# Performance work log

Hardware: AMD Instinct MI355X
Metric: run time of the kernel (lower is better)

## Reference

```python
import jax, jax.numpy as jnp
import numpy as np

N = 100000
E = 1600000
IN_DIM = 4
HIDDEN = 64
OUT = 32
HEADS = 4
NEG_SLOPE = 0.2


def setup_inputs() -> dict:
    key = jax.random.key(0)
    ks = jax.random.split(key, 12)
    C1 = HIDDEN // HEADS  # 16 per-head channels in conv1
    inp = {
        "x": jax.random.normal(ks[0], (N, IN_DIM), dtype=jnp.float32),
        "edge_index": jax.random.randint(ks[1], (2, E), 0, N, dtype=jnp.int64),
        # conv1 (GATv2, heads=4, out_channels=16, concat)
        "Wl1": jax.random.normal(ks[2], (IN_DIM, HEADS * C1), dtype=jnp.float32) * 0.3,
        "Wr1": jax.random.normal(ks[3], (IN_DIM, HEADS * C1), dtype=jnp.float32) * 0.3,
        "att1": jax.random.normal(ks[4], (HEADS, C1), dtype=jnp.float32) * 0.3,
        "b1": jax.random.normal(ks[5], (HEADS * C1,), dtype=jnp.float32) * 0.1,
        "g1": jnp.ones((HIDDEN,), dtype=jnp.float32),
        "be1": jnp.zeros((HIDDEN,), dtype=jnp.float32),
        # conv2 (GATv2, heads=1, out_channels=32)
        "Wl2": jax.random.normal(ks[6], (HIDDEN, OUT), dtype=jnp.float32) * 0.1,
        "Wr2": jax.random.normal(ks[7], (HIDDEN, OUT), dtype=jnp.float32) * 0.1,
        "att2": jax.random.normal(ks[8], (1, OUT), dtype=jnp.float32) * 0.3,
        "b2": jax.random.normal(ks[9], (OUT,), dtype=jnp.float32) * 0.1,
        "g2": jnp.ones((OUT,), dtype=jnp.float32),
        "be2": jnp.zeros((OUT,), dtype=jnp.float32),
    }
    return inp


def gatv2_conv(x, Wl, Wr, att, bias, src, dst, heads, out_ch):
    # x: [N, F_in]; lin_l for source messages, lin_r for target (PyG GATv2Conv defaults)
    xl = (x @ Wl).reshape(N, heads, out_ch)  # [N,H,C]
    xr = (x @ Wr).reshape(N, heads, out_ch)
    m = xl[src] + xr[dst]                                     # [E,H,C] gather
    e = jnp.sum(jax.nn.leaky_relu(m, NEG_SLOPE) * att, axis=-1)  # [E,H]
    # segment softmax over destination node
    emax = jax.ops.segment_max(e, dst, num_segments=N)        # [N,H]
    ee = jnp.exp(e - emax[dst])
    denom = jax.ops.segment_sum(ee, dst, num_segments=N)      # [N,H]
    alpha = ee / denom[dst]
    out = jax.ops.segment_sum(xl[src] * alpha[..., None], dst, num_segments=N)  # [N,H,C]
    return out.reshape(N, heads * out_ch) + bias


def layer_norm(x, gamma, beta, eps=1e-5):
    mu = jnp.mean(x, axis=-1, keepdims=True)
    var = jnp.var(x, axis=-1, keepdims=True)
    return (x - mu) * jax.lax.rsqrt(var + eps) * gamma + beta


def reference(x, edge_index, Wl1, Wr1, att1, b1, g1, be1, Wl2, Wr2, att2, b2, g2, be2):
    src, dst = edge_index[0], edge_index[1]
    h = gatv2_conv(x, Wl1, Wr1, att1, b1, src, dst, HEADS, HIDDEN // HEADS)
    h = jax.nn.elu(layer_norm(h, g1, be1))
    h = gatv2_conv(h, Wl2, Wr2, att2, b2, src, dst, 1, OUT)
    return layer_norm(h, g2, be2)
```

## Files before the change

### kernel.cpp

```cpp
#include <hip/hip_runtime.h>
#include <math.h>

#define NN 100000
#define NE 1600000
#define HID 64
#define OUTC 32
#define NBUCK 196
#define NPB 512
#define EPB 3125
#define MAXB 10240
#define LOG2E 1.44269504088896340736f

typedef float f32x2 __attribute__((ext_vector_type(2)));

__device__ __forceinline__ f32x2 pk_mul(f32x2 a, f32x2 b) {
    f32x2 r;
    asm("v_pk_mul_f32 %0, %1, %2" : "=v"(r) : "v"(a), "v"(b));
    return r;
}
__device__ __forceinline__ f32x2 pk_fma(f32x2 a, f32x2 b, f32x2 c) {
    f32x2 r;
    asm("v_pk_fma_f32 %0, %1, %2, %3" : "=v"(r) : "v"(a), "v"(b), "v"(c));
    return r;
}
__device__ __forceinline__ f32x2 pk_add(f32x2 a, f32x2 b) {
    f32x2 r;
    asm("v_pk_add_f32 %0, %1, %2" : "=v"(r) : "v"(a), "v"(b));
    return r;
}
__device__ __forceinline__ f32x2 pk_fma_blo(f32x2 x, f32x2 b, f32x2 c) {
    f32x2 r;
    asm("v_pk_fma_f32 %0, %1, %2, %3 op_sel:[0,0,0] op_sel_hi:[0,1,1]" : "=v"(r) : "v"(x), "v"(b), "v"(c));
    return r;
}
__device__ __forceinline__ f32x2 pk_fma_bhi(f32x2 x, f32x2 b, f32x2 c) {
    f32x2 r;
    asm("v_pk_fma_f32 %0, %1, %2, %3 op_sel:[1,0,0] op_sel_hi:[1,1,1]" : "=v"(r) : "v"(x), "v"(b), "v"(c));
    return r;
}
__device__ __forceinline__ f32x2 pk_mul_bhi(f32x2 x, f32x2 b) {
    f32x2 r;
    asm("v_pk_mul_f32 %0, %1, %2 op_sel:[1,0] op_sel_hi:[1,1]" : "=v"(r) : "v"(x), "v"(b));
    return r;
}
__device__ __forceinline__ f32x2 pk_abs(f32x2 a) {
    f32x2 r;
    r.x = __builtin_fabsf(a.x);
    r.y = __builtin_fabsf(a.y);
    return r;
}
__device__ __forceinline__ unsigned short f2bf(float f) {
    unsigned int u = __float_as_uint(f);
    u += 0x7FFFu + ((u >> 16) & 1u);
    return (unsigned short)(u >> 16);
}
__device__ __forceinline__ float quad_add_xor1(float v) {
    int t = __builtin_amdgcn_mov_dpp(__float_as_int(v), 0xB1, 0xF, 0xF, true);
    return v + __int_as_float(t);
}
__device__ __forceinline__ float quad_add_xor2(float v) {
    int t = __builtin_amdgcn_mov_dpp(__float_as_int(v), 0x4E, 0xF, 0xF, true);
    return v + __int_as_float(t);
}
__device__ __forceinline__ float ex2(float v) {
    float r;
    asm("v_exp_f32 %0, %1" : "=v"(r) : "v"(v));
    return r;
}


__global__ __launch_bounds__(256) void bucketB_kernel(const int* __restrict__ ei,
                                                      int* __restrict__ gcount,
                                                      unsigned int* __restrict__ staging) {
    __shared__ int cnt[NBUCK];
    __shared__ int cur[NBUCK];
    int tid = threadIdx.x;
    for (int i = tid; i < NBUCK; i += 256) cnt[i] = 0;
    __syncthreads();
    int base = blockIdx.x * EPB;
    const int* dstp = ei + NE;
    for (int i = tid; i < EPB; i += 256) atomicAdd(&cnt[dstp[base + i] >> 9], 1);
    __syncthreads();
    for (int i = tid; i < NBUCK; i += 256)
        cur[i] = i * MAXB + atomicAdd(&gcount[i], cnt[i]);
    __syncthreads();
    for (int i = tid; i < EPB; i += 256) {
        int d = dstp[base + i];
        int s = ei[base + i];
        int pos = atomicAdd(&cur[d >> 9], 1);
        staging[pos] = ((unsigned int)(d & 511) << 17) | (unsigned int)s;
    }
}

__global__ __launch_bounds__(256) void scanG_kernel(const int* __restrict__ gcount,
                                                    int* __restrict__ gbase) {
    __shared__ int sbuf[256];
    int tid = threadIdx.x;
    int v = (tid < NBUCK) ? gcount[tid] : 0;
    int run = v;
    sbuf[tid] = run;
    __syncthreads();
    for (int off = 1; off < 256; off <<= 1) {
        int u = (tid >= off) ? sbuf[tid - off] : 0;
        __syncthreads();
        run += u;
        sbuf[tid] = run;
        __syncthreads();
    }
    if (tid < NBUCK) gbase[tid] = run - v;
    if (tid == 0) gbase[NBUCK] = NE;
}

__global__ __launch_bounds__(256) void bucketC_kernel(const unsigned int* __restrict__ staging,
                                                      const int* __restrict__ gcount,
                                                      const int* __restrict__ gbase,
                                                      int* __restrict__ rowptr,
                                                      int* __restrict__ csr_src) {
    int b = blockIdx.x;
    int node0 = b << 9;
    int nnode = min(512, NN - node0);
    int ecnt = gcount[b];
    int e0 = gbase[b];
    const unsigned int* st = staging + (size_t)b * MAXB;
    __shared__ int deg[512];
    __shared__ int sbuf[256];
    int tid = threadIdx.x;
    deg[tid] = 0;
    deg[tid + 256] = 0;
    __syncthreads();
    for (int e = tid; e < ecnt; e += 256) atomicAdd(&deg[st[e] >> 17], 1);
    __syncthreads();
    int d0 = deg[2 * tid], d1 = deg[2 * tid + 1];
    int tsum = d0 + d1;
    int run = tsum;
    sbuf[tid] = tsum;
    __syncthreads();
    for (int off = 1; off < 256; off <<= 1) {
        int u = (tid >= off) ? sbuf[tid - off] : 0;
        __syncthreads();
        run += u;
        sbuf[tid] = run;
        __syncthreads();
    }
    int eb = run - tsum;
    deg[2 * tid] = eb;
    deg[2 * tid + 1] = eb + d0;
    if (2 * tid < nnode) rowptr[node0 + 2 * tid] = e0 + eb;
    if (2 * tid + 1 < nnode) rowptr[node0 + 2 * tid + 1] = e0 + eb + d0;
    if (b == NBUCK - 1 && tid == 0) rowptr[NN] = NE;
    __syncthreads();
    for (int e = tid; e < ecnt; e += 256) {
        unsigned int p = st[e];
        int dl = p >> 17;
        int src = (int)(p & 0x1FFFFu);
        int pos = e0 + atomicAdd(&deg[dl], 1);
        csr_src[pos] = src;
    }
}


#define PROC1(X, IDX, MASKED)                                                 \
    {                                                                         \
        f32x2 Xxy = {X.x, X.y}, Xzw = {X.z, X.w};                             \
        f32x2 s01 = pk_fma_blo(Xxy, wl0_01, pk_fma_bhi(Xxy, wl1_01,           \
                    pk_fma_blo(Xzw, wl2_01, pk_fma_bhi(Xzw, wl3_01, xr01)))); \
        f32x2 s23 = pk_fma_blo(Xxy, wl0_23, pk_fma_bhi(Xxy, wl1_23,           \
                    pk_fma_blo(Xzw, wl2_23, pk_fma_bhi(Xzw, wl3_23, xr23)))); \
        f32x2 t01 = pk_abs(s01), t23 = pk_abs(s23);                           \
        f32x2 dd = pk_fma(s01, a06_01, pk_fma(t01, a04_01,                    \
                   pk_fma(s23, a06_23, pk_mul(t23, a04_23))));                \
        float vv = dd.x + dd.y;                                               \
        vv = quad_add_xor1(vv);                                               \
        vv = quad_add_xor2(vv);   \
        float ev = ex2(vv);                                                   \
        if (MASKED && (IDX) >= cnt) ev = 0.f;                                 \
        ssum += ev;                                                           \
        f32x2 ev2 = {ev, ev};                                                 \
        accA = pk_fma(ev2, Xxy, accA);                                        \
        accB = pk_fma(ev2, Xzw, accB);                                        \
    }

__global__ __launch_bounds__(256) void gather1_kernel(const int* __restrict__ rowptr,
                                                      const int* __restrict__ csr_src,
                                                      const float* __restrict__ x,
                                                      const float* __restrict__ Wl,
                                                      const float* __restrict__ Wr,
                                                      const float* __restrict__ att,
                                                      const float* __restrict__ b1,
                                                      const float* __restrict__ g1,
                                                      const float* __restrict__ be1,
                                                      const float* __restrict__ Wl2,
                                                      const float* __restrict__ Wr2,
                                                      unsigned short* __restrict__ xl2b,
                                                      float* __restrict__ xr2) {
    __shared__ float sWl[4 * HID], sWr[4 * HID];
    __shared__ float satt[HID], sb[HID], sg[HID], sbe[HID];
    __shared__ float sW2[2 * HID * OUTC];
    __shared__ float sh[8 * HID];
    int tid = threadIdx.x;
    if (tid < 256) {
        sWl[tid] = Wl[tid];
        sWr[tid] = Wr[tid];
    }
    if (tid < HID) {
        satt[tid] = att[tid];
        sb[tid] = b1[tid];
        sg[tid] = g1[tid];
        sbe[tid] = be1[tid];
    }
    {
        const float4* wl4 = (const float4*)Wl2;
        const float4* wr4 = (const float4*)Wr2;
        float4* s4 = (float4*)sW2;
        for (int i = tid; i < 1024; i += 256)
            s4[i] = (i < 512) ? wl4[i] : wr4[i - 512];
    }
    __syncthreads();
    int hw = tid >> 5;
    int node = blockIdx.x * 8 + hw;
    int lane = tid & 63;
    int hbase = lane & 32;
    int ln = lane & 31;
    int grp = ln >> 4;
    int ch = (ln & 15) * 4;
    int p0 = rowptr[node], p1 = rowptr[node + 1];

    f32x2 wl0_01 = {sWl[ch + 0], sWl[ch + 1]},            wl0_23 = {sWl[ch + 2], sWl[ch + 3]};
    f32x2 wl1_01 = {sWl[64 + ch + 0], sWl[64 + ch + 1]},  wl1_23 = {sWl[64 + ch + 2], sWl[64 + ch + 3]};
    f32x2 wl2_01 = {sWl[128 + ch + 0], sWl[128 + ch + 1]}, wl2_23 = {sWl[128 + ch + 2], sWl[128 + ch + 3]};
    f32x2 wl3_01 = {sWl[192 + ch + 0], sWl[192 + ch + 1]}, wl3_23 = {sWl[192 + ch + 2], sWl[192 + ch + 3]};

    float4 xd = *(const float4*)(x + node * 4);
    f32x2 Dxy = {xd.x, xd.y}, Dzw = {xd.z, xd.w};
    f32x2 wr0_01 = {sWr[ch + 0], sWr[ch + 1]},            wr0_23 = {sWr[ch + 2], sWr[ch + 3]};
    f32x2 wr1_01 = {sWr[64 + ch + 0], sWr[64 + ch + 1]},  wr1_23 = {sWr[64 + ch + 2], sWr[64 + ch + 3]};
    f32x2 wr2_01 = {sWr[128 + ch + 0], sWr[128 + ch + 1]}, wr2_23 = {sWr[128 + ch + 2], sWr[128 + ch + 3]};
    f32x2 wr3_01 = {sWr[192 + ch + 0], sWr[192 + ch + 1]}, wr3_23 = {sWr[192 + ch + 2], sWr[192 + ch + 3]};
    f32x2 xr01 = pk_fma_blo(Dxy, wr0_01, pk_fma_bhi(Dxy, wr1_01,
                 pk_fma_blo(Dzw, wr2_01, pk_mul_bhi(Dzw, wr3_01))));
    f32x2 xr23 = pk_fma_blo(Dxy, wr0_23, pk_fma_bhi(Dxy, wr1_23,
                 pk_fma_blo(Dzw, wr2_23, pk_mul_bhi(Dzw, wr3_23))));

    f32x2 a06_01 = {0.6f * LOG2E * satt[ch + 0], 0.6f * LOG2E * satt[ch + 1]};
    f32x2 a06_23 = {0.6f * LOG2E * satt[ch + 2], 0.6f * LOG2E * satt[ch + 3]};
    f32x2 a04_01 = {0.4f * LOG2E * satt[ch + 0], 0.4f * LOG2E * satt[ch + 1]};
    f32x2 a04_23 = {0.4f * LOG2E * satt[ch + 2], 0.4f * LOG2E * satt[ch + 3]};

    const float4* x4 = (const float4*)x;
    float ssum = 0.f;
    f32x2 accA = {0.f, 0.f}, accB = {0.f, 0.f};
    for (int p = p0; p < p1; p += 32) {
        int cnt = min(32, p1 - p);
        int srcs = (ln < cnt) ? csr_src[p + ln] : 0;
        int j = 0;
        for (; j + 8 <= cnt; j += 8) {
            int s0 = __shfl(srcs, hbase + j + grp);
            int s1 = __shfl(srcs, hbase + j + 2 + grp);
            int s2 = __shfl(srcs, hbase + j + 4 + grp);
            int s3 = __shfl(srcs, hbase + j + 6 + grp);
            float4 X0 = x4[s0];
            float4 X1 = x4[s1];
            float4 X2 = x4[s2];
            float4 X3 = x4[s3];
            PROC1(X0, 0, 0)
            PROC1(X1, 0, 0)
            PROC1(X2, 0, 0)
            PROC1(X3, 0, 0)
        }
        for (; j < cnt; j += 2) {
            int idx = j + grp;
            int s0 = __shfl(srcs, hbase + (idx & 31));
            float4 X0 = x4[s0];
            PROC1(X0, idx, 1)
        }
    }
    float aA0 = accA.x, aA1 = accA.y, aB0 = accB.x, aB1 = accB.y;
    ssum += __shfl_xor(ssum, 16);
    aA0 += __shfl_xor(aA0, 16); aA1 += __shfl_xor(aA1, 16);
    aB0 += __shfl_xor(aB0, 16); aB1 += __shfl_xor(aB1, 16);
    f32x2 kA = {aA0, aA1}, kB = {aB0, aB1};
    f32x2 o01 = pk_fma_blo(kA, wl0_01, pk_fma_bhi(kA, wl1_01,
                pk_fma_blo(kB, wl2_01, pk_mul_bhi(kB, wl3_01))));
    f32x2 o23 = pk_fma_blo(kA, wl0_23, pk_fma_bhi(kA, wl1_23,
                pk_fma_blo(kB, wl2_23, pk_mul_bhi(kB, wl3_23))));
    float inv_s = (p1 > p0) ? __builtin_amdgcn_rcpf(ssum) : 0.f;
    float v0 = o01.x * inv_s + sb[ch + 0];
    float v1 = o01.y * inv_s + sb[ch + 1];
    float v2 = o23.x * inv_s + sb[ch + 2];
    float v3 = o23.y * inv_s + sb[ch + 3];
    float s4v = v0 + v1 + v2 + v3;
    s4v += __shfl_xor(s4v, 1); s4v += __shfl_xor(s4v, 2);
    s4v += __shfl_xor(s4v, 4); s4v += __shfl_xor(s4v, 8);
    float mu = s4v * (1.f / 64.f);
    float d0 = v0 - mu, d1 = v1 - mu, d2 = v2 - mu, d3 = v3 - mu;
    float q4 = d0 * d0 + d1 * d1 + d2 * d2 + d3 * d3;
    q4 += __shfl_xor(q4, 1); q4 += __shfl_xor(q4, 2);
    q4 += __shfl_xor(q4, 4); q4 += __shfl_xor(q4, 8);
    float inv = __builtin_amdgcn_rsqf(q4 * (1.f / 64.f) + 1e-5f);
    float y0 = d0 * inv * sg[ch + 0] + sbe[ch + 0];
    float y1 = d1 * inv * sg[ch + 1] + sbe[ch + 1];
    float y2 = d2 * inv * sg[ch + 2] + sbe[ch + 2];
    float y3 = d3 * inv * sg[ch + 3] + sbe[ch + 3];
    y0 = y0 > 0.f ? y0 : (ex2(y0 * LOG2E) - 1.f);
    y1 = y1 > 0.f ? y1 : (ex2(y1 * LOG2E) - 1.f);
    y2 = y2 > 0.f ? y2 : (ex2(y2 * LOG2E) - 1.f);
    y3 = y3 > 0.f ? y3 : (ex2(y3 * LOG2E) - 1.f);
    if (grp == 0) {
        *(float4*)(sh + hw * 64 + ch) = make_float4(y0, y1, y2, y3);
    }
    {
        int col = ln;
        float al = 0.f, ar = 0.f;
        const float* shp = sh + hw * 64;
#pragma unroll
        for (int k = 0; k < HID; k++) {
            float hv = shp[k];
            al += hv * sW2[k * 32 + col];
            ar += hv * sW2[HID * OUTC + k * 32 + col];
        }
        xl2b[node * 32 + col] = f2bf(al);
        xr2[node * 32 + col] = ar;
    }
}


#define G2_PROC(RV, IDX, MASKED)                                              \
    {                                                                         \
        f32x2 L01, L23, L45, L67;                                             \
        L01.x = __uint_as_float(RV.x << 16); L01.y = __uint_as_float(RV.x & 0xFFFF0000u); \
        L23.x = __uint_as_float(RV.y << 16); L23.y = __uint_as_float(RV.y & 0xFFFF0000u); \
        L45.x = __uint_as_float(RV.z << 16); L45.y = __uint_as_float(RV.z & 0xFFFF0000u); \
        L67.x = __uint_as_float(RV.w << 16); L67.y = __uint_as_float(RV.w & 0xFFFF0000u); \
        f32x2 s01 = pk_add(L01, xr01), s23 = pk_add(L23, xr23);               \
        f32x2 s45 = pk_add(L45, xr45), s67 = pk_add(L67, xr67);               \
        f32x2 t01 = pk_abs(s01), t23 = pk_abs(s23);                           \
        f32x2 t45 = pk_abs(s45), t67 = pk_abs(s67);                           \
        f32x2 dd = pk_fma(s01, a06_01, pk_fma(t01, a04_01,                    \
                   pk_fma(s23, a06_23, pk_fma(t23, a04_23,                    \
                   pk_fma(s45, a06_45, pk_fma(t45, a04_45,                    \
                   pk_fma(s67, a06_67, pk_mul(t67, a04_67))))))));            \
        float vv = dd.x + dd.y;                                               \
        vv = quad_add_xor1(vv);                                               \
        vv = quad_add_xor2(vv);   \
        float ev = ex2(vv);                                                   \
        if (MASKED && (IDX) >= cnt) ev = 0.f;                                 \
        ssum += ev;                                                           \
        f32x2 ev2 = {ev, ev};                                                 \
        ac01 = pk_fma(ev2, L01, ac01); ac23 = pk_fma(ev2, L23, ac23);         \
        ac45 = pk_fma(ev2, L45, ac45); ac67 = pk_fma(ev2, L67, ac67);         \
    }

__global__ __launch_bounds__(256) void gather2_kernel(const int* __restrict__ rowptr,
                                                      const int* __restrict__ csr_src,
                                                      const unsigned short* __restrict__ xl2b,
                                                      const float* __restrict__ xr2,
                                                      const float* __restrict__ att,
                                                      const float* __restrict__ b2,
                                                      const float* __restrict__ g2,
                                                      const float* __restrict__ be2,
                                                      float* __restrict__ out) {
    __shared__ float satt[OUTC], sb[OUTC], sg[OUTC], sbe[OUTC];
    int tid = threadIdx.x;
    if (tid < OUTC) {
        satt[tid] = att[tid];
        sb[tid] = b2[tid];
        sg[tid] = g2[tid];
        sbe[tid] = be2[tid];
    }
    __syncthreads();
    int node = blockIdx.x * 8 + (tid >> 5);
    int lane = tid & 63;
    int hbase = lane & 32;
    int ln = lane & 31;
    int es = ln >> 2;
    int ch = (ln & 3) * 8;
    int p0 = rowptr[node], p1 = rowptr[node + 1];

    const float* xrp = xr2 + (size_t)node * 32 + ch;
    float4 xra = *(const float4*)xrp;
    float4 xrb = *(const float4*)(xrp + 4);
    f32x2 xr01 = {xra.x, xra.y}, xr23 = {xra.z, xra.w};
    f32x2 xr45 = {xrb.x, xrb.y}, xr67 = {xrb.z, xrb.w};
    f32x2 a06_01 = {0.6f * LOG2E * satt[ch + 0], 0.6f * LOG2E * satt[ch + 1]};
    f32x2 a06_23 = {0.6f * LOG2E * satt[ch + 2], 0.6f * LOG2E * satt[ch + 3]};
    f32x2 a06_45 = {0.6f * LOG2E * satt[ch + 4], 0.6f * LOG2E * satt[ch + 5]};
    f32x2 a06_67 = {0.6f * LOG2E * satt[ch + 6], 0.6f * LOG2E * satt[ch + 7]};
    f32x2 a04_01 = {0.4f * LOG2E * satt[ch + 0], 0.4f * LOG2E * satt[ch + 1]};
    f32x2 a04_23 = {0.4f * LOG2E * satt[ch + 2], 0.4f * LOG2E * satt[ch + 3]};
    f32x2 a04_45 = {0.4f * LOG2E * satt[ch + 4], 0.4f * LOG2E * satt[ch + 5]};
    f32x2 a04_67 = {0.4f * LOG2E * satt[ch + 6], 0.4f * LOG2E * satt[ch + 7]};

    float ssum = 0.f;
    f32x2 ac01 = {0.f, 0.f}, ac23 = {0.f, 0.f}, ac45 = {0.f, 0.f}, ac67 = {0.f, 0.f};
    for (int p = p0; p < p1; p += 32) {
        int cnt = min(32, p1 - p);
        int srcs = (ln < cnt) ? csr_src[p + ln] : 0;
        int j = 0;
        for (; j + 8 <= cnt; j += 8) {
            int sa = __shfl(srcs, hbase + j + es);
            uint4 Ra = *(const uint4*)(xl2b + (size_t)sa * 32 + ch);
            G2_PROC(Ra, 0, 0)
        }
        if (j < cnt) {
            int idx = j + es;
            int sa = __shfl(srcs, hbase + (idx & 31));
            uint4 Ra = *(const uint4*)(xl2b + (size_t)sa * 32 + ch);
            G2_PROC(Ra, idx, 1)
        }
    }
    float A0 = ac01.x, A1 = ac01.y, A2 = ac23.x, A3 = ac23.y;
    float A4 = ac45.x, A5 = ac45.y, A6 = ac67.x, A7 = ac67.y;
    for (int off = 4; off < 32; off <<= 1) {
        ssum += __shfl_xor(ssum, off);
        A0 += __shfl_xor(A0, off); A1 += __shfl_xor(A1, off);
        A2 += __shfl_xor(A2, off); A3 += __shfl_xor(A3, off);
        A4 += __shfl_xor(A4, off); A5 += __shfl_xor(A5, off);
        A6 += __shfl_xor(A6, off); A7 += __shfl_xor(A7, off);
    }
    float inv_s = (p1 > p0) ? __builtin_amdgcn_rcpf(ssum) : 0.f;
    float v0 = A0 * inv_s + sb[ch + 0], v1 = A1 * inv_s + sb[ch + 1];
    float v2 = A2 * inv_s + sb[ch + 2], v3 = A3 * inv_s + sb[ch + 3];
    float v4 = A4 * inv_s + sb[ch + 4], v5 = A5 * inv_s + sb[ch + 5];
    float v6 = A6 * inv_s + sb[ch + 6], v7 = A7 * inv_s + sb[ch + 7];
    float s8 = v0 + v1 + v2 + v3 + v4 + v5 + v6 + v7;
    s8 += __shfl_xor(s8, 1); s8 += __shfl_xor(s8, 2);
    float mu = s8 * (1.f / 32.f);
    float d0 = v0 - mu, d1 = v1 - mu, d2 = v2 - mu, d3 = v3 - mu;
    float d4 = v4 - mu, d5 = v5 - mu, d6 = v6 - mu, d7 = v7 - mu;
    float q8 = d0 * d0 + d1 * d1 + d2 * d2 + d3 * d3 + d4 * d4 + d5 * d5 + d6 * d6 + d7 * d7;
    q8 += __shfl_xor(q8, 1); q8 += __shfl_xor(q8, 2);
    float inv = __builtin_amdgcn_rsqf(q8 * (1.f / 32.f) + 1e-5f);
    if (es == 0) {
        float4 oa, ob;
        oa.x = d0 * inv * sg[ch + 0] + sbe[ch + 0];
        oa.y = d1 * inv * sg[ch + 1] + sbe[ch + 1];
        oa.z = d2 * inv * sg[ch + 2] + sbe[ch + 2];
        oa.w = d3 * inv * sg[ch + 3] + sbe[ch + 3];
        ob.x = d4 * inv * sg[ch + 4] + sbe[ch + 4];
        ob.y = d5 * inv * sg[ch + 5] + sbe[ch + 5];
        ob.z = d6 * inv * sg[ch + 6] + sbe[ch + 6];
        ob.w = d7 * inv * sg[ch + 7] + sbe[ch + 7];
        *(float4*)(out + (size_t)node * 32 + ch) = oa;
        *(float4*)(out + (size_t)node * 32 + ch + 4) = ob;
    }
}

extern "C" void kernel_launch(void* const* d_in, const int* in_sizes, int n_in,
                              void* d_out, int out_size, void* d_ws, size_t ws_size,
                              hipStream_t stream) {
    const float* x    = (const float*)d_in[0];
    const int* ei     = (const int*)d_in[1];
    const float* Wl1  = (const float*)d_in[2];
    const float* Wr1  = (const float*)d_in[3];
    const float* att1 = (const float*)d_in[4];
    const float* b1   = (const float*)d_in[5];
    const float* g1   = (const float*)d_in[6];
    const float* be1  = (const float*)d_in[7];
    const float* Wl2  = (const float*)d_in[8];
    const float* Wr2  = (const float*)d_in[9];
    const float* att2 = (const float*)d_in[10];
    const float* b2   = (const float*)d_in[11];
    const float* g2   = (const float*)d_in[12];
    const float* be2  = (const float*)d_in[13];
    float* out = (float*)d_out;

    char* W = (char*)d_ws;
    unsigned short* xl2b = (unsigned short*)W;
    float* xr2 = (float*)(W + 6400000);
    int* rowptr = (int*)(W + 19200000);
    int* csr_src = rowptr + NN + 1;
    unsigned int* staging = (unsigned int*)(csr_src + NE);
    int* gcount = (int*)(staging + (size_t)NBUCK * MAXB);
    int* gbase = gcount + NBUCK;

    const int B = 256;

    hipMemsetAsync(gcount, 0, NBUCK * sizeof(int), stream);
    bucketB_kernel<<<NPB, B, 0, stream>>>(ei, gcount, staging);
    scanG_kernel<<<1, B, 0, stream>>>(gcount, gbase);
    bucketC_kernel<<<NBUCK, B, 0, stream>>>(staging, gcount, gbase, rowptr, csr_src);

    gather1_kernel<<<NN / 8, B, 0, stream>>>(rowptr, csr_src, x, Wl1, Wr1, att1,
                                             b1, g1, be1, Wl2, Wr2, xl2b, xr2);

    gather2_kernel<<<NN / 8, B, 0, stream>>>(rowptr, csr_src, xl2b, xr2, att2,
                                             b2, g2, be2, out);
}
```

Measured before the change: 163.2 us.

## Fold bucket-offset scan into bucketC and read layer-2 weights from global

Removes the single-block scanG kernel launch. Each bucketC block now computes its own edge offset with a shared-memory reduction over the preceding bucket counts. Separately, gather1 no longer stages the 16 KB Wl2/Wr2 matrices into LDS and reads them directly from global memory (cache-resident) with a partial unroll. This cuts per-block LDS footprint and staging loads, which may raise occupancy, at the cost of more global/cache traffic in the projection loop.

```diff
diff --git a/kernel.cpp b/kernel.cpp
--- a/kernel.cpp
+++ b/kernel.cpp
@@ -92,39 +92,27 @@
     }
 }
 
-__global__ __launch_bounds__(256) void scanG_kernel(const int* __restrict__ gcount,
-                                                    int* __restrict__ gbase) {
-    __shared__ int sbuf[256];
-    int tid = threadIdx.x;
-    int v = (tid < NBUCK) ? gcount[tid] : 0;
-    int run = v;
-    sbuf[tid] = run;
-    __syncthreads();
-    for (int off = 1; off < 256; off <<= 1) {
-        int u = (tid >= off) ? sbuf[tid - off] : 0;
-        __syncthreads();
-        run += u;
-        sbuf[tid] = run;
-        __syncthreads();
-    }
-    if (tid < NBUCK) gbase[tid] = run - v;
-    if (tid == 0) gbase[NBUCK] = NE;
-}
-
 __global__ __launch_bounds__(256) void bucketC_kernel(const unsigned int* __restrict__ staging,
                                                       const int* __restrict__ gcount,
-                                                      const int* __restrict__ gbase,
                                                       int* __restrict__ rowptr,
                                                       int* __restrict__ csr_src) {
     int b = blockIdx.x;
     int node0 = b << 9;
     int nnode = min(512, NN - node0);
-    int ecnt = gcount[b];
-    int e0 = gbase[b];
-    const unsigned int* st = staging + (size_t)b * MAXB;
+    int tid = threadIdx.x;
     __shared__ int deg[512];
     __shared__ int sbuf[256];
-    int tid = threadIdx.x;
+    int acc = (tid < b) ? gcount[tid] : 0;
+    sbuf[tid] = acc;
+    __syncthreads();
+    for (int off = 128; off >= 1; off >>= 1) {
+        if (tid < off) sbuf[tid] += sbuf[tid + off];
+        __syncthreads();
+    }
+    int e0 = sbuf[0];
+    int ecnt = gcount[b];
+    const unsigned int* st = staging + (size_t)b * MAXB;
+    __syncthreads();
     deg[tid] = 0;
     deg[tid + 256] = 0;
     __syncthreads();
@@ -195,7 +183,6 @@
                                                       float* __restrict__ xr2) {
     __shared__ float sWl[4 * HID], sWr[4 * HID];
     __shared__ float satt[HID], sb[HID], sg[HID], sbe[HID];
-    __shared__ float sW2[2 * HID * OUTC];
     __shared__ float sh[8 * HID];
     int tid = threadIdx.x;
     if (tid < 256) {
@@ -207,13 +194,6 @@
         sb[tid] = b1[tid];
         sg[tid] = g1[tid];
         sbe[tid] = be1[tid];
-    }
-    {
-        const float4* wl4 = (const float4*)Wl2;
-        const float4* wr4 = (const float4*)Wr2;
-        float4* s4 = (float4*)sW2;
-        for (int i = tid; i < 1024; i += 256)
-            s4[i] = (i < 512) ? wl4[i] : wr4[i - 512];
     }
     __syncthreads();
     int hw = tid >> 5;
@@ -312,11 +292,11 @@
         int col = ln;
         float al = 0.f, ar = 0.f;
         const float* shp = sh + hw * 64;
-#pragma unroll
+#pragma unroll 16
         for (int k = 0; k < HID; k++) {
             float hv = shp[k];
-            al += hv * sW2[k * 32 + col];
-            ar += hv * sW2[HID * OUTC + k * 32 + col];
+            al += hv * Wl2[k * 32 + col];
+            ar += hv * Wr2[k * 32 + col];
         }
         xl2b[node * 32 + col] = f2bf(al);
         xr2[node * 32 + col] = ar;
@@ -471,14 +451,12 @@
     int* csr_src = rowptr + NN + 1;
     unsigned int* staging = (unsigned int*)(csr_src + NE);
     int* gcount = (int*)(staging + (size_t)NBUCK * MAXB);
-    int* gbase = gcount + NBUCK;
 
     const int B = 256;
 
     hipMemsetAsync(gcount, 0, NBUCK * sizeof(int), stream);
     bucketB_kernel<<<NPB, B, 0, stream>>>(ei, gcount, staging);
-    scanG_kernel<<<1, B, 0, stream>>>(gcount, gbase);
-    bucketC_kernel<<<NBUCK, B, 0, stream>>>(staging, gcount, gbase, rowptr, csr_src);
+    bucketC_kernel<<<NBUCK, B, 0, stream>>>(staging, gcount, rowptr, csr_src);
 
     gather1_kernel<<<NN / 8, B, 0, stream>>>(rowptr, csr_src, x, Wl1, Wr1, att1,
                                              b1, g1, be1, Wl2, Wr2, xl2b, xr2);
```

Result: slower. 172.1 us (+5.4%).
